# Kernel optimization log

Hardware: AMD Instinct MI355X
Metric: run time of the kernel (lower is better)

Reference implementation:

```python
import jax, jax.numpy as jnp
import numpy as np


def setup_inputs() -> dict:
    key = jax.random.key(0)
    ks = jax.random.split(key, 7)
    T, I, H, O = 100000, 128, 512, 1
    s_ih = 1.0 / np.sqrt(H)
    return {
        "inputSequence": jax.random.normal(ks[0], (T, I), jnp.float32),
        "W_ih": jax.random.normal(ks[1], (4 * H, I), jnp.float32) * s_ih,
        "b_ih": jax.random.normal(ks[2], (4 * H,), jnp.float32) * s_ih,
        "W_hh": jax.random.normal(ks[3], (4 * H, H), jnp.float32) * s_ih,
        "b_hh": jax.random.normal(ks[4], (4 * H,), jnp.float32) * s_ih,
        "W_out": jax.random.normal(ks[5], (O, H), jnp.float32) * s_ih,
        "b_out": jax.random.normal(ks[6], (O,), jnp.float32) * s_ih,
    }


def reference(inputSequence, W_ih, b_ih, W_hh, b_hh, W_out, b_out):
    H = W_hh.shape[1]
    # Precompute input projection for all timesteps: [T, 4H]
    x_proj = inputSequence @ W_ih.T + (b_ih + b_hh)

    def step(carry, xp):
        h, c = carry
        gates = xp + W_hh @ h  # [4H], PyTorch gate order i,f,g,o
        i = jax.nn.sigmoid(gates[:H])
        f = jax.nn.sigmoid(gates[H:2 * H])
        g = jnp.tanh(gates[2 * H:3 * H])
        o = jax.nn.sigmoid(gates[3 * H:])
        c = f * c + i * g
        h = o * jnp.tanh(c)
        # dropout(p=0) is identity; linear + sigmoid, take element 0
        p = jax.nn.sigmoid(W_out @ h + b_out)[0]
        return (h, c), p

    h0 = jnp.zeros((H,), inputSequence.dtype)
    c0 = jnp.zeros((H,), inputSequence.dtype)
    (_, _), pAction = jax.lax.scan(step, (h0, c0), x_proj)
    return pAction
```

## Files before the change

### kernel.cpp

```cpp
#include <hip/hip_runtime.h>

#define T_STEPS 100000
#define NWG 32
#define TPB 512
#define HD 512
#define ID 128
#define UPW 16
#define ROWS 64

__global__ __launch_bounds__(TPB, 2) void lstm_persist(
    const float* __restrict__ x,
    const float* __restrict__ W_ih,
    const float* __restrict__ b_ih,
    const float* __restrict__ W_hh,
    const float* __restrict__ b_hh,
    const float* __restrict__ W_out,
    const float* __restrict__ b_out,
    float* __restrict__ out,
    unsigned long long* __restrict__ hpk)
{
  const int w    = blockIdx.x;
  const int tid  = threadIdx.x;
  const int wave = tid >> 6;
  const int lane = tid & 63;
  const int qr   = tid >> 3;
  const int c8   = tid & 7;

  __shared__ float h_lds[HD];
  __shared__ float part_lds[ROWS][65];
  __shared__ float gates_lds[ROWS];
  __shared__ float xp_lds[2][ROWS];
  __shared__ float bsum_lds[ROWS];

  float Whh[8][8];
  #pragma unroll
  for (int p = 0; p < 8; ++p) {
    const int q = wave*8 + p;
    const int R = (q>>4)*HD + UPW*w + (q&15);
    const float* src = W_hh + (size_t)R*HD + lane;
    #pragma unroll
    for (int j = 0; j < 8; ++j) Whh[p][j] = src[64*j];
  }
  float Wih[16];
  {
    const int R = (qr>>4)*HD + UPW*w + (qr&15);
    const float* src = W_ih + (size_t)R*ID + c8*16;
    #pragma unroll
    for (int i = 0; i < 16; ++i) Wih[i] = src[i];
  }
  float Wo[8];
  if (wave == 0) {
    #pragma unroll
    for (int j = 0; j < 8; ++j) Wo[j] = W_out[lane + 64*j];
  }
  const float bo = b_out[0];

  if (tid < ROWS) {
    const int R = (tid>>4)*HD + UPW*w + (tid&15);
    bsum_lds[tid] = b_ih[R] + b_hh[R];
  }
  __syncthreads();

  if (tid < UPW) {
    __hip_atomic_store(&hpk[UPW*w + tid], 0ull,
                       __ATOMIC_RELAXED, __HIP_MEMORY_SCOPE_AGENT);
  }

  {
    float s = 0.f;
    const float* xr = x + c8*16;
    #pragma unroll
    for (int i = 0; i < 16; ++i) s += Wih[i]*xr[i];
    s += __shfl_xor(s, 1); s += __shfl_xor(s, 2); s += __shfl_xor(s, 4);
    if (c8 == 0) xp_lds[0][qr] = s + bsum_lds[qr];
  }

  float creg = 0.f;

  for (int t = 1; t <= T_STEPS; ++t) {
    const unsigned int tag = (unsigned int)(t - 1);
    unsigned long long* sl = hpk + (size_t)((t - 1) & 1) * HD;

    unsigned long long v;
    unsigned int guard = 0;
    do {
      v = __hip_atomic_load(&sl[tid], __ATOMIC_RELAXED, __HIP_MEMORY_SCOPE_AGENT);
    } while ((unsigned int)(v >> 32) != tag && ++guard < (1u << 27));
    h_lds[tid] = __uint_as_float((unsigned int)v);
    __syncthreads();

    if (wave == 0 && t >= 2 && ((t - 2) & 31) == w) {
      float s = 0.f;
      #pragma unroll
      for (int j = 0; j < 8; ++j) s = fmaf(Wo[j], h_lds[lane + 64*j], s);
      s += __shfl_xor(s, 1);  s += __shfl_xor(s, 2);  s += __shfl_xor(s, 4);
      s += __shfl_xor(s, 8);  s += __shfl_xor(s, 16); s += __shfl_xor(s, 32);
      if (lane == 0) out[t - 2] = 1.f / (1.f + __expf(-(s + bo)));
    }

    float hreg[8];
    #pragma unroll
    for (int j = 0; j < 8; ++j) hreg[j] = h_lds[lane + 64*j];
    #pragma unroll
    for (int p = 0; p < 8; ++p) {
      float s = 0.f;
      #pragma unroll
      for (int j = 0; j < 8; ++j) s = fmaf(Whh[p][j], hreg[j], s);
      part_lds[wave*8 + p][lane] = s;
    }
    __syncthreads();

    {
      float s = 0.f;
      #pragma unroll
      for (int i = 0; i < 8; ++i) s += part_lds[qr][c8*8 + i];
      s += __shfl_xor(s, 1); s += __shfl_xor(s, 2); s += __shfl_xor(s, 4);
      if (c8 == 0) gates_lds[qr] = s + xp_lds[(t - 1) & 1][qr];
    }
    __syncthreads();

    if (tid < UPW) {
      const float ii = 1.f / (1.f + __expf(-gates_lds[tid]));
      const float ff = 1.f / (1.f + __expf(-gates_lds[16 + tid]));
      const float e2g = __expf(2.f * gates_lds[32 + tid]);
      const float gg = 1.f - 2.f / (e2g + 1.f);
      const float oo = 1.f / (1.f + __expf(-gates_lds[48 + tid]));
      creg = ff * creg + ii * gg;
      const float e2c = __expf(2.f * creg);
      const float hh = oo * (1.f - 2.f / (e2c + 1.f));
      const unsigned long long pk =
          ((unsigned long long)(unsigned int)t << 32) |
          (unsigned long long)__float_as_uint(hh);
      __hip_atomic_store(&hpk[(size_t)(t & 1) * HD + UPW*w + tid], pk,
                         __ATOMIC_RELAXED, __HIP_MEMORY_SCOPE_AGENT);
    }

    if (t < T_STEPS) {
      float s = 0.f;
      const float* xr = x + (size_t)t * ID + c8*16;
      #pragma unroll
      for (int i = 0; i < 16; ++i) s += Wih[i]*xr[i];
      s += __shfl_xor(s, 1); s += __shfl_xor(s, 2); s += __shfl_xor(s, 4);
      if (c8 == 0) xp_lds[t & 1][qr] = s + bsum_lds[qr];
    }
  }

  if (w == 0) {
    unsigned long long* sl = hpk + (size_t)(T_STEPS & 1) * HD;
    unsigned long long v;
    unsigned int guard = 0;
    do {
      v = __hip_atomic_load(&sl[tid], __ATOMIC_RELAXED, __HIP_MEMORY_SCOPE_AGENT);
    } while ((unsigned int)(v >> 32) != (unsigned int)T_STEPS && ++guard < (1u << 27));
    h_lds[tid] = __uint_as_float((unsigned int)v);
    __syncthreads();
    if (wave == 0) {
      float s = 0.f;
      #pragma unroll
      for (int j = 0; j < 8; ++j) s = fmaf(Wo[j], h_lds[lane + 64*j], s);
      s += __shfl_xor(s, 1);  s += __shfl_xor(s, 2);  s += __shfl_xor(s, 4);
      s += __shfl_xor(s, 8);  s += __shfl_xor(s, 16); s += __shfl_xor(s, 32);
      if (lane == 0) out[T_STEPS - 1] = 1.f / (1.f + __expf(-(s + bo)));
    }
  }
}

extern "C" void kernel_launch(void* const* d_in, const int* in_sizes, int n_in,
                              void* d_out, int out_size, void* d_ws, size_t ws_size,
                              hipStream_t stream) {
  (void)in_sizes; (void)n_in; (void)out_size; (void)ws_size;
  const float* x     = (const float*)d_in[0];
  const float* W_ih  = (const float*)d_in[1];
  const float* b_ih  = (const float*)d_in[2];
  const float* W_hh  = (const float*)d_in[3];
  const float* b_hh  = (const float*)d_in[4];
  const float* W_out = (const float*)d_in[5];
  const float* b_out = (const float*)d_in[6];
  float* out = (float*)d_out;
  unsigned long long* hpk = (unsigned long long*)d_ws;

  lstm_persist<<<NWG, TPB, 0, stream>>>(x, W_ih, b_ih, W_hh, b_hh,
                                        W_out, b_out, out, hpk);
}
```

Measured before the change: 178.6 ms.

## Co-locate persistent workgroups on one XCC and sync through shared L2 atomics

Launches many workgroups and has each read its hardware XCC id. Only the first 32 that land on a single chosen XCC take part; the rest exit. A handshake then checks that L2-coherent atomic reads and writes (atomic or/swap without system scope) are visible to all participants, and if so the per-step hidden-state exchange uses them instead of device-scope atomics. The goal is to cut cross-die coherence latency on every one of the 100k recurrent steps. The cost is a launch of 1024 blocks, a memset, handshake overhead and reliance on undocumented XCC placement and cache behaviour, with a fallback to the old slow path.

```diff
diff --git a/kernel.cpp b/kernel.cpp
--- a/kernel.cpp
+++ b/kernel.cpp
@@ -1,12 +1,51 @@
 #include <hip/hip_runtime.h>
 
 #define T_STEPS 100000
-#define NWG 32
+#define NLAUNCH 1024
+#define NPART 32
 #define TPB 512
 #define HD 512
 #define ID 128
 #define UPW 16
 #define ROWS 64
+#define GUARD_MAIN (1u << 23)
+#define HS_SPIN    (1u << 16)
+#define OK_SPIN    (1u << 22)
+
+#define CTRL_OFF 1024
+#define HS_OFF   1025
+#define OK_OFF   1057
+#define WS_CLEAR ((OK_OFF + 32) * 8)
+
+__device__ inline unsigned long long l2_read(unsigned long long* p) {
+  unsigned long long old; unsigned long long zero = 0;
+  asm volatile("global_atomic_or_x2 %0, %1, %2, off sc0\n\ts_waitcnt vmcnt(0)"
+               : "=&v"(old) : "v"(p), "v"(zero) : "memory");
+  return old;
+}
+__device__ inline void l2_write(unsigned long long* p, unsigned long long v) {
+  asm volatile("global_atomic_swap_x2 %0, %1, off" :: "v"(p), "v"(v) : "memory");
+}
+__device__ inline unsigned long long dev_read(unsigned long long* p) {
+  return __hip_atomic_load(p, __ATOMIC_RELAXED, __HIP_MEMORY_SCOPE_AGENT);
+}
+__device__ inline void dev_write(unsigned long long* p, unsigned long long v) {
+  __hip_atomic_store(p, v, __ATOMIC_RELAXED, __HIP_MEMORY_SCOPE_AGENT);
+}
+
+__device__ inline unsigned long long poll_tag(unsigned long long* p, unsigned int tag,
+                                              bool fast, bool& dead) {
+  unsigned long long v;
+  if (!dead) {
+    unsigned int g = 0;
+    do { v = fast ? l2_read(p) : dev_read(p); }
+    while ((unsigned int)(v >> 32) != tag && ++g < GUARD_MAIN);
+    if (g >= GUARD_MAIN) dead = true;
+  } else {
+    v = fast ? l2_read(p) : dev_read(p);
+  }
+  return v;
+}
 
 __global__ __launch_bounds__(TPB, 2) void lstm_persist(
     const float* __restrict__ x,
@@ -17,20 +56,72 @@
     const float* __restrict__ W_out,
     const float* __restrict__ b_out,
     float* __restrict__ out,
-    unsigned long long* __restrict__ hpk)
+    unsigned long long* __restrict__ ws)
 {
-  const int w    = blockIdx.x;
+  unsigned long long* hpk = ws;
+  unsigned int* ctrl = (unsigned int*)(ws + CTRL_OFF);
+
   const int tid  = threadIdx.x;
   const int wave = tid >> 6;
   const int lane = tid & 63;
   const int qr   = tid >> 3;
   const int c8   = tid & 7;
 
+  __shared__ int role_sh;
+  __shared__ unsigned int cnt_sh;
   __shared__ float h_lds[HD];
   __shared__ float part_lds[ROWS][65];
   __shared__ float gates_lds[ROWS];
   __shared__ float xp_lds[2][ROWS];
   __shared__ float bsum_lds[ROWS];
+
+  unsigned int xcc;
+  asm volatile("s_getreg_b32 %0, hwreg(HW_REG_XCC_ID)" : "=s"(xcc));
+  if (tid == 0) {
+    int role = -1;
+    unsigned int prev = atomicCAS(&ctrl[0], 0u, xcc + 1u);
+    unsigned int chosen = (prev == 0u) ? xcc : (prev - 1u);
+    if (xcc == chosen) {
+      unsigned int idx = atomicAdd(&ctrl[1], 1u);
+      if (idx < NPART) role = (int)idx;
+    }
+    role_sh = role;
+  }
+  __syncthreads();
+  const int w = role_sh;
+  if (w < 0) return;
+
+  bool fast;
+  {
+    if (tid == 0) {
+      cnt_sh = 0;
+      l2_write(&ws[HS_OFF + w],
+               0xC0DEC0DE00000000ull | (unsigned long long)(w + 1));
+    }
+    __syncthreads();
+    if (tid < NPART) {
+      const unsigned long long want =
+          0xC0DEC0DE00000000ull | (unsigned long long)(tid + 1);
+      unsigned int g = 0;
+      while (l2_read(&ws[HS_OFF + tid]) != want && ++g < HS_SPIN) {}
+      if (g < HS_SPIN) atomicAdd(&cnt_sh, 1u);
+    }
+    __syncthreads();
+    const bool all_ok = (cnt_sh == NPART);
+    __syncthreads();
+    if (tid == 0) {
+      cnt_sh = 0;
+      dev_write(&ws[OK_OFF + w], all_ok ? 1ull : 2ull);
+    }
+    __syncthreads();
+    if (tid < NPART) {
+      unsigned long long v; unsigned int g = 0;
+      do { v = dev_read(&ws[OK_OFF + tid]); } while (v == 0ull && ++g < OK_SPIN);
+      if (v == 1ull) atomicAdd(&cnt_sh, 1u);
+    }
+    __syncthreads();
+    fast = (cnt_sh == NPART);
+  }
 
   float Whh[8][8];
   #pragma unroll
@@ -61,10 +152,6 @@
   }
   __syncthreads();
 
-  if (tid < UPW) {
-    __hip_atomic_store(&hpk[UPW*w + tid], 0ull,
-                       __ATOMIC_RELAXED, __HIP_MEMORY_SCOPE_AGENT);
-  }
 
   {
     float s = 0.f;
@@ -76,20 +163,17 @@
   }
 
   float creg = 0.f;
+  bool dead = false;
 
   for (int t = 1; t <= T_STEPS; ++t) {
     const unsigned int tag = (unsigned int)(t - 1);
     unsigned long long* sl = hpk + (size_t)((t - 1) & 1) * HD;
 
-    unsigned long long v;
-    unsigned int guard = 0;
-    do {
-      v = __hip_atomic_load(&sl[tid], __ATOMIC_RELAXED, __HIP_MEMORY_SCOPE_AGENT);
-    } while ((unsigned int)(v >> 32) != tag && ++guard < (1u << 27));
+    const unsigned long long v = poll_tag(&sl[tid], tag, fast, dead);
     h_lds[tid] = __uint_as_float((unsigned int)v);
     __syncthreads();
 
-    if (wave == 0 && t >= 2 && ((t - 2) & 31) == w) {
+    if (wave == 0 && t >= 2 && ((t - 2) & (NPART - 1)) == w) {
       float s = 0.f;
       #pragma unroll
       for (int j = 0; j < 8; ++j) s = fmaf(Wo[j], h_lds[lane + 64*j], s);
@@ -131,8 +215,8 @@
       const unsigned long long pk =
           ((unsigned long long)(unsigned int)t << 32) |
           (unsigned long long)__float_as_uint(hh);
-      __hip_atomic_store(&hpk[(size_t)(t & 1) * HD + UPW*w + tid], pk,
-                         __ATOMIC_RELAXED, __HIP_MEMORY_SCOPE_AGENT);
+      unsigned long long* dst = &hpk[(size_t)(t & 1) * HD + UPW*w + tid];
+      if (fast) l2_write(dst, pk); else dev_write(dst, pk);
     }
 
     if (t < T_STEPS) {
@@ -147,11 +231,8 @@
 
   if (w == 0) {
     unsigned long long* sl = hpk + (size_t)(T_STEPS & 1) * HD;
-    unsigned long long v;
-    unsigned int guard = 0;
-    do {
-      v = __hip_atomic_load(&sl[tid], __ATOMIC_RELAXED, __HIP_MEMORY_SCOPE_AGENT);
-    } while ((unsigned int)(v >> 32) != (unsigned int)T_STEPS && ++guard < (1u << 27));
+    const unsigned long long v =
+        poll_tag(&sl[tid], (unsigned int)T_STEPS, fast, dead);
     h_lds[tid] = __uint_as_float((unsigned int)v);
     __syncthreads();
     if (wave == 0) {
@@ -177,8 +258,10 @@
   const float* W_out = (const float*)d_in[5];
   const float* b_out = (const float*)d_in[6];
   float* out = (float*)d_out;
-  unsigned long long* hpk = (unsigned long long*)d_ws;
-
-  lstm_persist<<<NWG, TPB, 0, stream>>>(x, W_ih, b_ih, W_hh, b_hh,
-                                        W_out, b_out, out, hpk);
-}
+  unsigned long long* ws = (unsigned long long*)d_ws;
+
+  hipMemsetAsync(d_ws, 0, WS_CLEAR, stream);
+
+  lstm_persist<<<NLAUNCH, TPB, 0, stream>>>(x, W_ih, b_ih, W_hh, b_hh,
+                                            W_out, b_out, out, ws);
+}
```

Measured after the change: 258.2 ms. 44.6% more time.

## Restructure recurrent matvec so each lane owns a contiguous 64-wide row slice

Applied to the files above, without the earlier changes.

Each thread now holds 64 contiguous W_hh weights for one gate row and reads h as float4 from a double-buffered LDS tile. Each row's sum is reduced with three shuffles, which removes the part_lds scratch array and one barrier per step. The output projection moves after the h publish so it is off the critical path. The mailbox is now zeroed with a host memset, and a dead flag skips repeated spin timeouts. The cost is 64 weight registers per thread instead of 64 spread across 8 rows, and float4 LDS reads with possible bank conflicts.

```diff
diff --git a/kernel.cpp b/kernel.cpp
--- a/kernel.cpp
+++ b/kernel.cpp
@@ -7,6 +7,14 @@
 #define ID 128
 #define UPW 16
 #define ROWS 64
+#define GUARD (1u << 27)
+
+__device__ inline unsigned long long dev_read(unsigned long long* p) {
+  return __hip_atomic_load(p, __ATOMIC_RELAXED, __HIP_MEMORY_SCOPE_AGENT);
+}
+__device__ inline void dev_write(unsigned long long* p, unsigned long long v) {
+  __hip_atomic_store(p, v, __ATOMIC_RELAXED, __HIP_MEMORY_SCOPE_AGENT);
+}
 
 __global__ __launch_bounds__(TPB, 2) void lstm_persist(
     const float* __restrict__ x,
@@ -17,105 +25,97 @@
     const float* __restrict__ W_out,
     const float* __restrict__ b_out,
     float* __restrict__ out,
-    unsigned long long* __restrict__ hpk)
+    unsigned long long* __restrict__ mbx)
 {
   const int w    = blockIdx.x;
   const int tid  = threadIdx.x;
-  const int wave = tid >> 6;
-  const int lane = tid & 63;
+  const int v    = tid >> 6;
+  const int l    = tid & 63;
+  const int q    = v * 8 + (l >> 3);
+  const int k8   = l & 7;
   const int qr   = tid >> 3;
   const int c8   = tid & 7;
 
-  __shared__ float h_lds[HD];
-  __shared__ float part_lds[ROWS][65];
+  __shared__ float h_lds[2][8][68];
   __shared__ float gates_lds[ROWS];
   __shared__ float xp_lds[2][ROWS];
   __shared__ float bsum_lds[ROWS];
 
-  float Whh[8][8];
-  #pragma unroll
-  for (int p = 0; p < 8; ++p) {
-    const int q = wave*8 + p;
-    const int R = (q>>4)*HD + UPW*w + (q&15);
-    const float* src = W_hh + (size_t)R*HD + lane;
+  const int G = (q >> 4) * HD + UPW * w + (q & 15);
+
+  float Whh[64];
+  {
+    const float* src = W_hh + (size_t)G * HD + 64 * k8;
     #pragma unroll
-    for (int j = 0; j < 8; ++j) Whh[p][j] = src[64*j];
+    for (int jj = 0; jj < 16; ++jj) {
+      const float4 t4 = *reinterpret_cast<const float4*>(src + 4 * jj);
+      Whh[4*jj]   = t4.x; Whh[4*jj+1] = t4.y;
+      Whh[4*jj+2] = t4.z; Whh[4*jj+3] = t4.w;
+    }
   }
   float Wih[16];
   {
-    const int R = (qr>>4)*HD + UPW*w + (qr&15);
-    const float* src = W_ih + (size_t)R*ID + c8*16;
+    const int R = (qr >> 4) * HD + UPW * w + (qr & 15);
+    const float* src = W_ih + (size_t)R * ID + c8 * 16;
     #pragma unroll
     for (int i = 0; i < 16; ++i) Wih[i] = src[i];
   }
   float Wo[8];
-  if (wave == 0) {
+  if (v == 1) {
     #pragma unroll
-    for (int j = 0; j < 8; ++j) Wo[j] = W_out[lane + 64*j];
+    for (int j = 0; j < 8; ++j) Wo[j] = W_out[l + 64 * j];
   }
   const float bo = b_out[0];
 
   if (tid < ROWS) {
-    const int R = (tid>>4)*HD + UPW*w + (tid&15);
+    const int R = (tid >> 4) * HD + UPW * w + (tid & 15);
     bsum_lds[tid] = b_ih[R] + b_hh[R];
   }
   __syncthreads();
 
-  if (tid < UPW) {
-    __hip_atomic_store(&hpk[UPW*w + tid], 0ull,
-                       __ATOMIC_RELAXED, __HIP_MEMORY_SCOPE_AGENT);
-  }
 
   {
     float s = 0.f;
-    const float* xr = x + c8*16;
+    const float* xr = x + c8 * 16;
     #pragma unroll
-    for (int i = 0; i < 16; ++i) s += Wih[i]*xr[i];
+    for (int i = 0; i < 16; ++i) s += Wih[i] * xr[i];
     s += __shfl_xor(s, 1); s += __shfl_xor(s, 2); s += __shfl_xor(s, 4);
     if (c8 == 0) xp_lds[0][qr] = s + bsum_lds[qr];
   }
 
   float creg = 0.f;
+  bool dead = false;
 
   for (int t = 1; t <= T_STEPS; ++t) {
     const unsigned int tag = (unsigned int)(t - 1);
-    unsigned long long* sl = hpk + (size_t)((t - 1) & 1) * HD;
+    const int p = (t - 1) & 1;
+    unsigned long long* sl = mbx + (size_t)p * HD;
 
-    unsigned long long v;
-    unsigned int guard = 0;
-    do {
-      v = __hip_atomic_load(&sl[tid], __ATOMIC_RELAXED, __HIP_MEMORY_SCOPE_AGENT);
-    } while ((unsigned int)(v >> 32) != tag && ++guard < (1u << 27));
-    h_lds[tid] = __uint_as_float((unsigned int)v);
-    __syncthreads();
-
-    if (wave == 0 && t >= 2 && ((t - 2) & 31) == w) {
-      float s = 0.f;
-      #pragma unroll
-      for (int j = 0; j < 8; ++j) s = fmaf(Wo[j], h_lds[lane + 64*j], s);
-      s += __shfl_xor(s, 1);  s += __shfl_xor(s, 2);  s += __shfl_xor(s, 4);
-      s += __shfl_xor(s, 8);  s += __shfl_xor(s, 16); s += __shfl_xor(s, 32);
-      if (lane == 0) out[t - 2] = 1.f / (1.f + __expf(-(s + bo)));
+    unsigned long long pv;
+    if (!dead) {
+      unsigned int g = 0;
+      do { pv = dev_read(&sl[tid]); }
+      while ((unsigned int)(pv >> 32) != tag && ++g < GUARD);
+      if (g >= GUARD) dead = true;
+    } else {
+      pv = dev_read(&sl[tid]);
     }
-
-    float hreg[8];
-    #pragma unroll
-    for (int j = 0; j < 8; ++j) hreg[j] = h_lds[lane + 64*j];
-    #pragma unroll
-    for (int p = 0; p < 8; ++p) {
-      float s = 0.f;
-      #pragma unroll
-      for (int j = 0; j < 8; ++j) s = fmaf(Whh[p][j], hreg[j], s);
-      part_lds[wave*8 + p][lane] = s;
-    }
+    h_lds[p][tid >> 6][tid & 63] = __uint_as_float((unsigned int)pv);
     __syncthreads();
 
     {
       float s = 0.f;
+      const float* hrow = &h_lds[p][k8][0];
       #pragma unroll
-      for (int i = 0; i < 8; ++i) s += part_lds[qr][c8*8 + i];
+      for (int jj = 0; jj < 16; ++jj) {
+        const float4 h4 = *reinterpret_cast<const float4*>(hrow + 4 * jj);
+        s = fmaf(Whh[4*jj],   h4.x, s);
+        s = fmaf(Whh[4*jj+1], h4.y, s);
+        s = fmaf(Whh[4*jj+2], h4.z, s);
+        s = fmaf(Whh[4*jj+3], h4.w, s);
+      }
       s += __shfl_xor(s, 1); s += __shfl_xor(s, 2); s += __shfl_xor(s, 4);
-      if (c8 == 0) gates_lds[qr] = s + xp_lds[(t - 1) & 1][qr];
+      if ((l & 7) == 0) gates_lds[q] = s + xp_lds[p][q];
     }
     __syncthreads();
 
@@ -131,36 +131,48 @@
       const unsigned long long pk =
           ((unsigned long long)(unsigned int)t << 32) |
           (unsigned long long)__float_as_uint(hh);
-      __hip_atomic_store(&hpk[(size_t)(t & 1) * HD + UPW*w + tid], pk,
-                         __ATOMIC_RELAXED, __HIP_MEMORY_SCOPE_AGENT);
+      dev_write(&mbx[(size_t)(t & 1) * HD + UPW * w + tid], pk);
+    }
+
+    if (v == 1 && t >= 2 && ((t - 2) & (NWG - 1)) == w) {
+      float s = 0.f;
+      #pragma unroll
+      for (int j = 0; j < 8; ++j) s = fmaf(Wo[j], h_lds[p][j][l], s);
+      s += __shfl_xor(s, 1);  s += __shfl_xor(s, 2);  s += __shfl_xor(s, 4);
+      s += __shfl_xor(s, 8);  s += __shfl_xor(s, 16); s += __shfl_xor(s, 32);
+      if (l == 0) out[t - 2] = 1.f / (1.f + __expf(-(s + bo)));
     }
 
     if (t < T_STEPS) {
       float s = 0.f;
-      const float* xr = x + (size_t)t * ID + c8*16;
+      const float* xr = x + (size_t)t * ID + c8 * 16;
       #pragma unroll
-      for (int i = 0; i < 16; ++i) s += Wih[i]*xr[i];
+      for (int i = 0; i < 16; ++i) s += Wih[i] * xr[i];
       s += __shfl_xor(s, 1); s += __shfl_xor(s, 2); s += __shfl_xor(s, 4);
       if (c8 == 0) xp_lds[t & 1][qr] = s + bsum_lds[qr];
     }
   }
 
   if (w == 0) {
-    unsigned long long* sl = hpk + (size_t)(T_STEPS & 1) * HD;
-    unsigned long long v;
-    unsigned int guard = 0;
-    do {
-      v = __hip_atomic_load(&sl[tid], __ATOMIC_RELAXED, __HIP_MEMORY_SCOPE_AGENT);
-    } while ((unsigned int)(v >> 32) != (unsigned int)T_STEPS && ++guard < (1u << 27));
-    h_lds[tid] = __uint_as_float((unsigned int)v);
+    const int p = T_STEPS & 1;
+    unsigned long long* sl = mbx + (size_t)p * HD;
+    unsigned long long pv;
+    if (!dead) {
+      unsigned int g = 0;
+      do { pv = dev_read(&sl[tid]); }
+      while ((unsigned int)(pv >> 32) != (unsigned int)T_STEPS && ++g < GUARD);
+    } else {
+      pv = dev_read(&sl[tid]);
+    }
+    h_lds[p][tid >> 6][tid & 63] = __uint_as_float((unsigned int)pv);
     __syncthreads();
-    if (wave == 0) {
+    if (v == 1) {
       float s = 0.f;
       #pragma unroll
-      for (int j = 0; j < 8; ++j) s = fmaf(Wo[j], h_lds[lane + 64*j], s);
+      for (int j = 0; j < 8; ++j) s = fmaf(Wo[j], h_lds[p][j][l], s);
       s += __shfl_xor(s, 1);  s += __shfl_xor(s, 2);  s += __shfl_xor(s, 4);
       s += __shfl_xor(s, 8);  s += __shfl_xor(s, 16); s += __shfl_xor(s, 32);
-      if (lane == 0) out[T_STEPS - 1] = 1.f / (1.f + __expf(-(s + bo)));
+      if (l == 0) out[T_STEPS - 1] = 1.f / (1.f + __expf(-(s + bo)));
     }
   }
 }
@@ -177,8 +189,10 @@
   const float* W_out = (const float*)d_in[5];
   const float* b_out = (const float*)d_in[6];
   float* out = (float*)d_out;
-  unsigned long long* hpk = (unsigned long long*)d_ws;
+  unsigned long long* mbx = (unsigned long long*)d_ws;
+
+  hipMemsetAsync(d_ws, 0, 2 * HD * sizeof(unsigned long long), stream);
 
   lstm_persist<<<NWG, TPB, 0, stream>>>(x, W_ih, b_ih, W_hh, b_hh,
-                                        W_out, b_out, out, hpk);
+                                        W_out, b_out, out, mbx);
 }
```

Measured after the change: 184.3 ms. 1.03x slower.
